# Performance work log

Measured on AMD Instinct MI355X. Metric: run time of the kernel, lower is better.

Reference implementation:

```python
import jax, jax.numpy as jnp
import numpy as np

N_PTS = 1048576
N_SPHERES = 128
K_SMOOTH = 32.0
CLAMP_MIN = 1e-6


def setup_inputs() -> dict:
    key = jax.random.key(0)
    k1, k2, k3 = jax.random.split(key, 3)
    p = jax.random.normal(k1, (N_PTS, 3), dtype=jnp.float32)
    centers = 0.3 * jax.random.uniform(k2, (N_SPHERES, 3), dtype=jnp.float32) - 0.15
    radii = 0.2 * jax.random.uniform(k3, (N_SPHERES,), dtype=jnp.float32) - 0.1
    tfs = jnp.zeros((N_SPHERES, 3, 3), dtype=jnp.float32)
    return {"p": p, "centers": centers, "radii": radii, "tfs": tfs}


def reference(p, centers, radii, tfs):
    # tfs + identity: per-sphere rigid-ish transform
    tfs_full = tfs + jnp.eye(3, dtype=tfs.dtype)  # [n, 3, 3]
    # q[i, b, :] = tfs_full[i] @ p[b] - centers[i]   -> [n, N, 3]
    q = jnp.einsum('ijk,bk->ibj', tfs_full, p) - centers[:, None, :]
    # signed distance to each sphere: [n, N]
    sd = jnp.linalg.norm(q, axis=-1) - radii[:, None]
    # smooth_min over sphere axis (dim 0), k=32
    s = jnp.sum(jnp.exp(-K_SMOOTH * sd), axis=0)  # [N]
    out = -jnp.log(jnp.clip(s, CLAMP_MIN)) / K_SMOOTH
    return out[..., None]  # [N, 1]
```

## Files before the change

kernel.cpp:

```cpp
#include <hip/hip_runtime.h>
#include <math.h>

#if __has_builtin(__builtin_amdgcn_exp2f)
#define EXP2F __builtin_amdgcn_exp2f
#else
#define EXP2F exp2f
#endif
#if __has_builtin(__builtin_amdgcn_logf)
#define LOG2FF __builtin_amdgcn_logf
#else
#define LOG2FF log2f
#endif
#if __has_builtin(__builtin_amdgcn_sqrtf)
#define SQRTFF __builtin_amdgcn_sqrtf
#else
#define SQRTFF sqrtf
#endif

#define K_SMOOTH 32.0f
#define LOG2E 1.4426950408889634f
#define LN2 0.6931471805599453f
#define CLAMP_MIN 1e-6f
#define FAR_OUT 0.43173470493638357f

constexpr int NS_MAX = 128;
constexpr int BLOCK = 256;
constexpr int CPTS = 8;
constexpr int PTS_PER_BLOCK = BLOCK * CPTS;

__global__ __launch_bounds__(BLOCK) void smoothed_spheres_kernel(
    const float* __restrict__ p, const float* __restrict__ centers,
    const float* __restrict__ radii, const float* __restrict__ tfs,
    float* __restrict__ out, int n_pts, int n_spheres) {
  __shared__ float4 sph_ce[NS_MAX];
  __shared__ float  sph_T[NS_MAX][9];
  __shared__ int    queue[PTS_PER_BLOCK];
  __shared__ int    qcount;
  __shared__ float  redC[BLOCK / 64], redF[BLOCK / 64];
  __shared__ float  s_pthr2;
  __shared__ int    s_ident;

  const int tid = threadIdx.x;
  const int ns = (n_spheres < NS_MAX) ? n_spheres : NS_MAX;

  float candC = 0.0f;
  float candF = 0.0f;
  if (tid < ns) {
    const float cx = centers[3 * tid + 0];
    const float cy = centers[3 * tid + 1];
    const float cz = centers[3 * tid + 2];
    const float r = radii[tid];
    float fro = 0.0f;
#pragma unroll
    for (int j = 0; j < 9; ++j) {
      const float v = tfs[9 * tid + j];
      fro += v * v;
      sph_T[tid][j] = v + ((j == 0 || j == 4 || j == 8) ? 1.0f : 0.0f);
    }
    candC = SQRTFF(cx * cx + cy * cy + cz * cz) + r;
    candF = SQRTFF(fro);
    sph_ce[tid] = make_float4(cx, cy, cz, K_SMOOTH * LOG2E * r);
  }
  if (tid == 0) qcount = 0;

#pragma unroll
  for (int off = 32; off > 0; off >>= 1) {
    candC = fmaxf(candC, __shfl_xor(candC, off));
    candF = fmaxf(candF, __shfl_xor(candF, off));
  }
  if ((tid & 63) == 0) { redC[tid >> 6] = candC; redF[tid >> 6] = candF; }
  __syncthreads();
  if (tid == 0) {
    float Cmax = redC[0], Fmax = redF[0];
#pragma unroll
    for (int w = 1; w < BLOCK / 64; ++w) {
      Cmax = fmaxf(Cmax, redC[w]);
      Fmax = fmaxf(Fmax, redF[w]);
    }
    s_ident = (Fmax == 0.0f) ? 1 : 0;
    const float sd_req = logf((float)(ns > 0 ? ns : 1) * 1e6f) * (1.0f / K_SMOOTH) + 0.01f;
    if (Fmax < 1.0f) {
      const float pthr = (Cmax + sd_req) / (1.0f - Fmax);
      s_pthr2 = pthr * pthr;
    } else {
      s_pthr2 = 3.0e38f;
    }
  }
  __syncthreads();

  const int base = blockIdx.x * PTS_PER_BLOCK;
  const float pthr2 = s_pthr2;
#pragma unroll
  for (int j = 0; j < CPTS; ++j) {
    const int idx = base + j * BLOCK + tid;
    if (idx < n_pts) {
      const float px = p[3 * idx + 0];
      const float py = p[3 * idx + 1];
      const float pz = p[3 * idx + 2];
      const float pn2 = fmaf(px, px, fmaf(py, py, pz * pz));
      if (pn2 > pthr2) {
        out[idx] = FAR_OUT;
      } else {
        const int q = atomicAdd(&qcount, 1);
        queue[q] = idx;
      }
    }
  }
  __syncthreads();
  const int qn = qcount;

  if (s_ident) {
    for (int qi = tid; qi < qn; qi += BLOCK) {
      const int idx = queue[qi];
      const float px = p[3 * idx + 0];
      const float py = p[3 * idx + 1];
      const float pz = p[3 * idx + 2];
      float s = 0.0f;
#pragma unroll 4
      for (int i = 0; i < ns; ++i) {
        const float4 c = sph_ce[i];
        const float dx = px - c.x;
        const float dy = py - c.y;
        const float dz = pz - c.z;
        const float d2 = fmaf(dx, dx, fmaf(dy, dy, dz * dz));
        const float nq = SQRTFF(d2);
        s += EXP2F(fmaf(nq, -K_SMOOTH * LOG2E, c.w));
      }
      s = fmaxf(s, CLAMP_MIN);
      out[idx] = -LOG2FF(s) * (LN2 / K_SMOOTH);
    }
  } else {
    for (int qi = tid; qi < qn; qi += BLOCK) {
      const int idx = queue[qi];
      const float px = p[3 * idx + 0];
      const float py = p[3 * idx + 1];
      const float pz = p[3 * idx + 2];
      float s = 0.0f;
      for (int i = 0; i < ns; ++i) {
        const float4 c = sph_ce[i];
        const float* T = sph_T[i];
        const float qx = fmaf(T[0], px, fmaf(T[1], py, fmaf(T[2], pz, -c.x)));
        const float qy = fmaf(T[3], px, fmaf(T[4], py, fmaf(T[5], pz, -c.y)));
        const float qz = fmaf(T[6], px, fmaf(T[7], py, fmaf(T[8], pz, -c.z)));
        const float d2 = fmaf(qx, qx, fmaf(qy, qy, qz * qz));
        const float nq = SQRTFF(d2);
        s += EXP2F(fmaf(nq, -K_SMOOTH * LOG2E, c.w));
      }
      s = fmaxf(s, CLAMP_MIN);
      out[idx] = -LOG2FF(s) * (LN2 / K_SMOOTH);
    }
  }
}

extern "C" void kernel_launch(void* const* d_in, const int* in_sizes, int n_in,
                              void* d_out, int out_size, void* d_ws, size_t ws_size,
                              hipStream_t stream) {
  const float* p = (const float*)d_in[0];
  const float* centers = (const float*)d_in[1];
  const float* radii = (const float*)d_in[2];
  const float* tfs = (const float*)d_in[3];
  float* out = (float*)d_out;

  const int n_pts = in_sizes[0] / 3;
  const int n_spheres = in_sizes[2];

  const int grid = (n_pts + PTS_PER_BLOCK - 1) / PTS_PER_BLOCK;
  smoothed_spheres_kernel<<<grid, BLOCK, 0, stream>>>(p, centers, radii, tfs,
                                                      out, n_pts, n_spheres);
}
```

Baseline: 80.64 us.

## Store point coords in LDS queue, halve points per block, dual accumulators

The compaction queue now holds each near point's coordinates together with its index as a float4, so the compute loop no longer reloads p from global memory with a gather. Points per block drop from 8×256 to 4×256, which doubles the grid and keeps LDS usage within budget now that queue entries are 16 bytes. The identity-transform sphere loop is split into two independent accumulators with a larger unroll to shorten the add dependency chain. The trade-off is more blocks, each repeating the per-block sphere setup and threshold reduction, and changed float summation order.

```diff
diff --git a/kernel.cpp b/kernel.cpp
--- a/kernel.cpp
+++ b/kernel.cpp
@@ -25,7 +25,7 @@
 
 constexpr int NS_MAX = 128;
 constexpr int BLOCK = 256;
-constexpr int CPTS = 8;
+constexpr int CPTS = 4;
 constexpr int PTS_PER_BLOCK = BLOCK * CPTS;
 
 __global__ __launch_bounds__(BLOCK) void smoothed_spheres_kernel(
@@ -34,7 +34,7 @@
     float* __restrict__ out, int n_pts, int n_spheres) {
   __shared__ float4 sph_ce[NS_MAX];
   __shared__ float  sph_T[NS_MAX][9];
-  __shared__ int    queue[PTS_PER_BLOCK];
+  __shared__ float4 queue[PTS_PER_BLOCK];
   __shared__ int    qcount;
   __shared__ float  redC[BLOCK / 64], redF[BLOCK / 64];
   __shared__ float  s_pthr2;
@@ -102,7 +102,7 @@
         out[idx] = FAR_OUT;
       } else {
         const int q = atomicAdd(&qcount, 1);
-        queue[q] = idx;
+        queue[q] = make_float4(px, py, pz, __int_as_float(idx));
       }
     }
   }
@@ -111,30 +111,45 @@
 
   if (s_ident) {
     for (int qi = tid; qi < qn; qi += BLOCK) {
-      const int idx = queue[qi];
-      const float px = p[3 * idx + 0];
-      const float py = p[3 * idx + 1];
-      const float pz = p[3 * idx + 2];
-      float s = 0.0f;
-#pragma unroll 4
-      for (int i = 0; i < ns; ++i) {
-        const float4 c = sph_ce[i];
+      const float4 e = queue[qi];
+      const int idx = __float_as_int(e.w);
+      const float px = e.x, py = e.y, pz = e.z;
+      float s0 = 0.0f, s1 = 0.0f;
+#pragma unroll 8
+      for (int i = 0; i < ns; i += 2) {
+        {
+          const float4 c = sph_ce[i];
+          const float dx = px - c.x;
+          const float dy = py - c.y;
+          const float dz = pz - c.z;
+          const float d2 = fmaf(dx, dx, fmaf(dy, dy, dz * dz));
+          s0 += EXP2F(fmaf(SQRTFF(d2), -K_SMOOTH * LOG2E, c.w));
+        }
+        {
+          const float4 c = sph_ce[i + 1];
+          const float dx = px - c.x;
+          const float dy = py - c.y;
+          const float dz = pz - c.z;
+          const float d2 = fmaf(dx, dx, fmaf(dy, dy, dz * dz));
+          s1 += EXP2F(fmaf(SQRTFF(d2), -K_SMOOTH * LOG2E, c.w));
+        }
+      }
+      if (ns & 1) {
+        const float4 c = sph_ce[ns - 1];
         const float dx = px - c.x;
         const float dy = py - c.y;
         const float dz = pz - c.z;
         const float d2 = fmaf(dx, dx, fmaf(dy, dy, dz * dz));
-        const float nq = SQRTFF(d2);
-        s += EXP2F(fmaf(nq, -K_SMOOTH * LOG2E, c.w));
+        s0 += EXP2F(fmaf(SQRTFF(d2), -K_SMOOTH * LOG2E, c.w));
       }
-      s = fmaxf(s, CLAMP_MIN);
+      const float s = fmaxf(s0 + s1, CLAMP_MIN);
       out[idx] = -LOG2FF(s) * (LN2 / K_SMOOTH);
     }
   } else {
     for (int qi = tid; qi < qn; qi += BLOCK) {
-      const int idx = queue[qi];
-      const float px = p[3 * idx + 0];
-      const float py = p[3 * idx + 1];
-      const float pz = p[3 * idx + 2];
+      const float4 e = queue[qi];
+      const int idx = __float_as_int(e.w);
+      const float px = e.x, py = e.y, pz = e.z;
       float s = 0.0f;
       for (int i = 0; i < ns; ++i) {
         const float4 c = sph_ce[i];
@@ -143,8 +158,7 @@
         const float qy = fmaf(T[3], px, fmaf(T[4], py, fmaf(T[5], pz, -c.y)));
         const float qz = fmaf(T[6], px, fmaf(T[7], py, fmaf(T[8], pz, -c.z)));
         const float d2 = fmaf(qx, qx, fmaf(qy, qy, qz * qz));
-        const float nq = SQRTFF(d2);
-        s += EXP2F(fmaf(nq, -K_SMOOTH * LOG2E, c.w));
+        s += EXP2F(fmaf(SQRTFF(d2), -K_SMOOTH * LOG2E, c.w));
       }
       s = fmaxf(s, CLAMP_MIN);
       out[idx] = -LOG2FF(s) * (LN2 / K_SMOOTH);
```

Result: faster. 74.65 us (-7.4%).
